# Performance work log

Hardware: AMD Instinct MI355X
Metric: run time of the kernel (lower is better)

The kernel has to match this reference:

```python
import jax, jax.numpy as jnp
import numpy as np

SEQ_LEN, INPUT_DIM, HIDDEN_DIM, OUTPUT_DIM = 512, 512, 1024, 512
BATCH = 64


def setup_inputs() -> dict:
    key = jax.random.key(0)
    k1, k2, k3, k4, k5 = jax.random.split(key, 5)
    fan_in_i2h = INPUT_DIM + HIDDEN_DIM
    s1 = 1.0 / np.sqrt(fan_in_i2h)
    s2 = 1.0 / np.sqrt(HIDDEN_DIM)
    return {
        "x": jax.random.normal(k1, (BATCH, SEQ_LEN, INPUT_DIM), dtype=jnp.float32),
        # i2h: Linear(input_dim+hidden_dim, 4*hidden_dim); stored as (in, out) for x @ W
        "W_i2h": jax.random.uniform(k2, (fan_in_i2h, 4 * HIDDEN_DIM), minval=-s1, maxval=s1, dtype=jnp.float32),
        "b_i2h": jax.random.uniform(k3, (4 * HIDDEN_DIM,), minval=-s1, maxval=s1, dtype=jnp.float32),
        # h2o: Linear(hidden_dim, output_dim)
        "W_h2o": jax.random.uniform(k4, (HIDDEN_DIM, OUTPUT_DIM), minval=-s2, maxval=s2, dtype=jnp.float32),
        "b_h2o": jax.random.uniform(k5, (OUTPUT_DIM,), minval=-s2, maxval=s2, dtype=jnp.float32),
    }


def reference(x, W_i2h, b_i2h, W_h2o, b_h2o):
    B = x.shape[0]
    H = W_h2o.shape[0]
    h0 = jnp.zeros((B, H), dtype=x.dtype)
    c0 = jnp.zeros((B, H), dtype=x.dtype)

    def step(carry, x_t):
        h_t, c_t = carry
        combined = jnp.concatenate([x_t, h_t], axis=1)  # [B, in+H]
        gates = combined @ W_i2h + b_i2h                # [B, 4H]
        i_t, f_t, g_t, o_t = jnp.split(gates, 4, axis=1)
        i_t = jax.nn.sigmoid(i_t)
        f_t = jax.nn.sigmoid(f_t)
        g_t = jnp.tanh(g_t)
        o_t = jax.nn.sigmoid(o_t)
        c_new = f_t * c_t + i_t * g_t
        h_new = o_t * jnp.tanh(c_new)
        return (h_new, c_new), None

    # scan over time: x [B, T, in] -> [T, B, in]
    (h_last, _), _ = jax.lax.scan(step, (h0, c0), jnp.swapaxes(x, 0, 1))
    # original returns only the last timestep's output projection
    return h_last @ W_h2o + b_h2o
```

## Files before the change

kernel.cpp:

```cpp
#include <hip/hip_runtime.h>
#include <hip/hip_bf16.h>
#include <stdint.h>


typedef __bf16 bf16x8 __attribute__((ext_vector_type(8)));
typedef float  f32x4  __attribute__((ext_vector_type(4)));
typedef unsigned long long u64;

#define NWG   256
#define NTHR  512

#define WS_FLAGS  0
#define WS_GOMB   1024
#define WS_HBUF   17408
#define HB_STRIDE 262144
#define HB_LO     131072
#define WS_HLAST  (WS_HBUF + 2*HB_STRIDE)

#define L_WHI   0
#define L_WLO   49152
#define L_EXCH  98304
#define L_EXCH2 102400
#define LDS_BYTES 106496

__device__ __forceinline__ float sigm(float x) {
    return __builtin_amdgcn_rcpf(1.0f + __expf(-x));
}
__device__ __forceinline__ float tanh_f(float x) {
    x = fminf(fmaxf(x, -20.0f), 20.0f);
    float e = __expf(-2.0f * x);
    return (1.0f - e) * __builtin_amdgcn_rcpf(1.0f + e);
}

__global__ void lstm_init(char* __restrict__ ws) {
    int id = blockIdx.x * 256 + threadIdx.x;
    for (int i = id; i < 69888; i += 256 * 256)
        __hip_atomic_store((unsigned*)ws + i, 0u,
                           __ATOMIC_RELAXED, __HIP_MEMORY_SCOPE_AGENT);
}

__global__ __launch_bounds__(NTHR) void lstm_main(
        const float* __restrict__ x, const float* __restrict__ Wi2h,
        const float* __restrict__ bi2h, const float* __restrict__ Wh2o,
        const float* __restrict__ bh2o, float* __restrict__ out,
        char* __restrict__ ws) {
    extern __shared__ char lds[];
    const int tid = threadIdx.x, wg = blockIdx.x;
    const int w = tid >> 6, lane = tid & 63, g = lane >> 4, nl = lane & 15;
    const int mt = w & 3, kh = w >> 2;

    for (int u = tid; u < 3072; u += NTHR) {
        int ak = u >> 4, cl = u & 15;
        int n = (cl >> 2) * 1024 + wg * 4 + (cl & 3);
        bf16x8 hi8, lo8;
#pragma unroll
        for (int j = 0; j < 8; ++j) {
            float v = Wi2h[(size_t)(ak * 8 + j) * 4096 + n];
            __bf16 h = (__bf16)v;
            hi8[j] = h;
            lo8[j] = (__bf16)(v - (float)h);
        }
        *(bf16x8*)(lds + L_WHI + (size_t)u * 16) = hi8;
        *(bf16x8*)(lds + L_WLO + (size_t)u * 16) = lo8;
    }
    const float bias_nl = bi2h[(nl >> 2) * 1024 + wg * 4 + (nl & 3)];
    __syncthreads();

    unsigned* flags = (unsigned*)(ws + WS_FLAGS);
    unsigned* my_mb = (unsigned*)(ws + WS_GOMB) + wg * 16;
    float* exch  = (float*)(lds + L_EXCH);
    float* exch2 = (float*)(lds + L_EXCH2);
    float creg = 0.f;

#pragma unroll 1
    for (int t = 0; t < 512; ++t) {
        const char* hb_rd = ws + WS_HBUF + (size_t)(t & 1) * HB_STRIDE;
        char*       hb_wr = ws + WS_HBUF + (size_t)((t + 1) & 1) * HB_STRIDE;
        f32x4 acc0 = {0.f, 0.f, 0.f, 0.f}, acc1 = {0.f, 0.f, 0.f, 0.f};

        {
            const float* xb = x + ((size_t)(mt * 16 + nl) * 512 + t) * 512 + g * 8;
            const int s0 = kh * 8;
#pragma unroll
            for (int si = 0; si < 8; ++si) {
                const int s = s0 + si;
                float4 v0 = *(const float4*)(xb + s * 32);
                float4 v1 = *(const float4*)(xb + s * 32 + 4);
                float vv[8] = {v0.x, v0.y, v0.z, v0.w, v1.x, v1.y, v1.z, v1.w};
                bf16x8 ahi, alo;
#pragma unroll
                for (int j = 0; j < 8; ++j) {
                    __bf16 h = (__bf16)vv[j];
                    ahi[j] = h;
                    alo[j] = (__bf16)(vv[j] - (float)h);
                }
                const char* bp = lds + (size_t)(4 * s + g) * 256 + nl * 16;
                bf16x8 bhi = *(const bf16x8*)(bp + L_WHI);
                bf16x8 blo = *(const bf16x8*)(bp + L_WLO);
                if (s & 1) {
                    acc1 = __builtin_amdgcn_mfma_f32_16x16x32_bf16(ahi, bhi, acc1, 0, 0, 0);
                    acc1 = __builtin_amdgcn_mfma_f32_16x16x32_bf16(ahi, blo, acc1, 0, 0, 0);
                    acc1 = __builtin_amdgcn_mfma_f32_16x16x32_bf16(alo, bhi, acc1, 0, 0, 0);
                } else {
                    acc0 = __builtin_amdgcn_mfma_f32_16x16x32_bf16(ahi, bhi, acc0, 0, 0, 0);
                    acc0 = __builtin_amdgcn_mfma_f32_16x16x32_bf16(ahi, blo, acc0, 0, 0, 0);
                    acc0 = __builtin_amdgcn_mfma_f32_16x16x32_bf16(alo, bhi, acc0, 0, 0, 0);
                }
            }
        }

        if (tid == 0) {
            while (__hip_atomic_load(my_mb, __ATOMIC_RELAXED,
                                     __HIP_MEMORY_SCOPE_AGENT) < (unsigned)t) {}
        }
        __syncthreads();

        {
            const int s0 = 16 + kh * 16;
#pragma unroll 8
            for (int si = 0; si < 16; ++si) {
                const int s = s0 + si;
                size_t ha = ((size_t)(mt * 32 + (s - 16)) * 64 + lane) * 16;
                const char* bse = hb_rd + ha;
                u64 q0 = __hip_atomic_load((const u64*)(bse),
                           __ATOMIC_RELAXED, __HIP_MEMORY_SCOPE_AGENT);
                u64 q1 = __hip_atomic_load((const u64*)(bse + 8),
                           __ATOMIC_RELAXED, __HIP_MEMORY_SCOPE_AGENT);
                u64 q2 = __hip_atomic_load((const u64*)(bse + HB_LO),
                           __ATOMIC_RELAXED, __HIP_MEMORY_SCOPE_AGENT);
                u64 q3 = __hip_atomic_load((const u64*)(bse + HB_LO + 8),
                           __ATOMIC_RELAXED, __HIP_MEMORY_SCOPE_AGENT);
                union { u64 q[2]; bf16x8 v; } uh, ul;
                uh.q[0] = q0; uh.q[1] = q1;
                ul.q[0] = q2; ul.q[1] = q3;
                bf16x8 ahi = uh.v, alo = ul.v;
                const char* bp = lds + (size_t)(4 * s + g) * 256 + nl * 16;
                bf16x8 bhi = *(const bf16x8*)(bp + L_WHI);
                bf16x8 blo = *(const bf16x8*)(bp + L_WLO);
                if (s & 1) {
                    acc1 = __builtin_amdgcn_mfma_f32_16x16x32_bf16(ahi, bhi, acc1, 0, 0, 0);
                    acc1 = __builtin_amdgcn_mfma_f32_16x16x32_bf16(ahi, blo, acc1, 0, 0, 0);
                    acc1 = __builtin_amdgcn_mfma_f32_16x16x32_bf16(alo, bhi, acc1, 0, 0, 0);
                } else {
                    acc0 = __builtin_amdgcn_mfma_f32_16x16x32_bf16(ahi, bhi, acc0, 0, 0, 0);
                    acc0 = __builtin_amdgcn_mfma_f32_16x16x32_bf16(ahi, blo, acc0, 0, 0, 0);
                    acc0 = __builtin_amdgcn_mfma_f32_16x16x32_bf16(alo, bhi, acc0, 0, 0, 0);
                }
            }
        }

        if (kh == 1) {
#pragma unroll
            for (int j = 0; j < 4; ++j)
                exch[mt * 256 + (g * 4 + j) * 16 + nl] = acc0[j] + acc1[j];
        }
        __syncthreads();
        if (kh == 0) {
#pragma unroll
            for (int j = 0; j < 4; ++j) {
                float pre = acc0[j] + acc1[j] + exch[mt * 256 + (g * 4 + j) * 16 + nl]
                          + bias_nl;
                float act = ((nl >> 2) == 2) ? tanh_f(pre) : sigm(pre);
                exch2[mt * 256 + (g * 4 + j) * 16 + nl] = act;
            }
        }
        __syncthreads();
        if (tid < 256) {
            int mt2 = tid >> 6, r = (tid >> 2) & 15, hc = tid & 3;
            const float* a2 = exch2 + mt2 * 256 + r * 16;
            float iv = a2[hc], fv = a2[4 + hc], gv = a2[8 + hc], ov = a2[12 + hc];
            float cc = fv * creg + iv * gv;
            creg = cc;
            float hv = ov * tanh_f(cc);
            __bf16 hh = (__bf16)hv;
            __bf16 hl = (__bf16)(hv - (float)hh);
            int k = 512 + wg * 4 + hc;
            int hs = (k >> 5) - 16, kg = (k >> 3) & 3, j8 = k & 7;
            uint32_t ad = ((uint32_t)(mt2 * 32 + hs) * 64 + kg * 16 + r) * 16 + j8 * 2;
            __hip_atomic_store((unsigned short*)(hb_wr + ad),
                               __builtin_bit_cast(unsigned short, hh),
                               __ATOMIC_RELAXED, __HIP_MEMORY_SCOPE_AGENT);
            __hip_atomic_store((unsigned short*)(hb_wr + HB_LO + ad),
                               __builtin_bit_cast(unsigned short, hl),
                               __ATOMIC_RELAXED, __HIP_MEMORY_SCOPE_AGENT);
            if (t == 511)
                __hip_atomic_store((float*)(ws + WS_HLAST)
                                       + (mt2 * 16 + r) * 1024 + wg * 4 + hc, hv,
                                   __ATOMIC_RELAXED, __HIP_MEMORY_SCOPE_AGENT);
        }
        __syncthreads();
        if (tid == 0)
            __hip_atomic_store(&flags[wg], (unsigned)(t + 1),
                               __ATOMIC_RELAXED, __HIP_MEMORY_SCOPE_AGENT);
        if (wg == 0 && w == 0) {
            unsigned tgt = (unsigned)(t + 1);
            const u64* f64 = (const u64*)flags;
            for (;;) {
                u64 a = __hip_atomic_load(f64 + 2 * lane,
                          __ATOMIC_RELAXED, __HIP_MEMORY_SCOPE_AGENT);
                u64 b = __hip_atomic_load(f64 + 2 * lane + 1,
                          __ATOMIC_RELAXED, __HIP_MEMORY_SCOPE_AGENT);
                unsigned m0 = min(min((unsigned)a, (unsigned)(a >> 32)),
                                  min((unsigned)b, (unsigned)(b >> 32)));
                if (__all(m0 >= tgt)) break;
            }
            unsigned* mb = (unsigned*)(ws + WS_GOMB);
#pragma unroll
            for (int q = 0; q < 4; ++q)
                __hip_atomic_store(mb + (q * 64 + lane) * 16, tgt,
                                   __ATOMIC_RELAXED, __HIP_MEMORY_SCOPE_AGENT);
        }
    }

    if (tid == 0) {
        while (__hip_atomic_load(my_mb, __ATOMIC_RELAXED,
                                 __HIP_MEMORY_SCOPE_AGENT) < 512u) {}
    }
    __syncthreads();
    __builtin_amdgcn_fence(__ATOMIC_ACQUIRE, "agent");

    const float* HL = (const float*)(ws + WS_HLAST);
    float* hl = (float*)lds;
    float* pp = (float*)(lds + 8192);
    int bb = wg & 63, q = wg >> 6;
    hl[tid]       = HL[bb * 1024 + tid];
    hl[tid + 512] = HL[bb * 1024 + 512 + tid];
    __syncthreads();
    int c = q * 128 + (tid & 127), kq = tid >> 7;
    const float* wc = Wh2o + c;
    float part = 0.f;
#pragma unroll 8
    for (int k = kq * 256; k < kq * 256 + 256; ++k)
        part += hl[k] * wc[(size_t)k * 512];
    pp[kq * 128 + (tid & 127)] = part;
    __syncthreads();
    if (tid < 128)
        out[bb * 512 + q * 128 + tid] =
            pp[tid] + pp[128 + tid] + pp[256 + tid] + pp[384 + tid] + bh2o[q * 128 + tid];
}

extern "C" void kernel_launch(void* const* d_in, const int* in_sizes, int n_in,
                              void* d_out, int out_size, void* d_ws, size_t ws_size,
                              hipStream_t stream) {
    const float* x    = (const float*)d_in[0];
    const float* Wi2h = (const float*)d_in[1];
    const float* bi2h = (const float*)d_in[2];
    const float* Wh2o = (const float*)d_in[3];
    const float* bh2o = (const float*)d_in[4];
    float* out = (float*)d_out;
    char* ws = (char*)d_ws;

    hipFuncSetAttribute(reinterpret_cast<const void*>(lstm_main),
                        hipFuncAttributeMaxDynamicSharedMemorySize, LDS_BYTES);

    lstm_init<<<256, 256, 0, stream>>>(ws);

    void* args[] = {(void*)&x, (void*)&Wi2h, (void*)&bi2h, (void*)&Wh2o,
                    (void*)&bh2o, (void*)&out, (void*)&ws};
    hipLaunchCooperativeKernel(reinterpret_cast<void*>(lstm_main),
                               dim3(NWG), dim3(NTHR), args, LDS_BYTES, stream);
}
```

Before: 5.293 ms.

## Stage recurrent h state per-XCD with cooperative copy and pipelined loads

Each workgroup finds its XCC id and a slot within that XCD. Per step, the 32 workgroups on an XCD each copy a slice of the global h buffer into an XCD-local staging buffer, then synchronise through a per-XCD counter and flag. The MFMA pass then reads h from the staging buffer with sc0 loads issued in software-pipelined batches, and half of the x-projection work is moved between the copy and the wait to hide latency. This aims to cut cross-XCD coherent traffic for h reads, at the cost of an extra per-XCD barrier, and it assumes exactly 32 workgroups land on each XCD.

```diff
diff --git a/kernel.cpp b/kernel.cpp
--- a/kernel.cpp
+++ b/kernel.cpp
@@ -10,12 +10,17 @@
 #define NWG   256
 #define NTHR  512
 
-#define WS_FLAGS  0
-#define WS_GOMB   1024
-#define WS_HBUF   17408
-#define HB_STRIDE 262144
-#define HB_LO     131072
-#define WS_HLAST  (WS_HBUF + 2*HB_STRIDE)
+#define WS_FLAGS   0
+#define WS_GOMB    1024
+#define WS_XCDC    17408
+#define WS_SCNT    17920
+#define WS_SFLAG   18432
+#define WS_HBUF    20480
+#define HB_STRIDE  262144
+#define HB_LO      131072
+#define WS_HLAST   544768
+#define WS_STAGE   806912
+#define STG_STRIDE 262144
 
 #define L_WHI   0
 #define L_WLO   49152
@@ -34,12 +39,77 @@
 
 __global__ void lstm_init(char* __restrict__ ws) {
     int id = blockIdx.x * 256 + threadIdx.x;
-    for (int i = id; i < 69888; i += 256 * 256)
+    for (int i = id; i < 136192; i += 256 * 256)
         __hip_atomic_store((unsigned*)ws + i, 0u,
                            __ATOMIC_RELAXED, __HIP_MEMORY_SCOPE_AGENT);
 }
 
-__global__ __launch_bounds__(NTHR) void lstm_main(
+#define X_HALF(A)                                                              \
+  { _Pragma("unroll")                                                          \
+    for (int si = (A); si < (A) + 4; ++si) {                                   \
+      const int s = kh * 8 + si;                                               \
+      float4 v0 = *(const float4*)(xb + s * 32);                               \
+      float4 v1 = *(const float4*)(xb + s * 32 + 4);                           \
+      float vv[8] = {v0.x, v0.y, v0.z, v0.w, v1.x, v1.y, v1.z, v1.w};          \
+      bf16x8 ahi, alo;                                                         \
+      _Pragma("unroll")                                                        \
+      for (int j = 0; j < 8; ++j) {                                            \
+        __bf16 hh_ = (__bf16)vv[j];                                            \
+        ahi[j] = hh_;                                                          \
+        alo[j] = (__bf16)(vv[j] - (float)hh_);                                 \
+      }                                                                        \
+      const char* bp = lds + (size_t)(4 * s + g) * 256 + nl * 16;              \
+      bf16x8 bhi = *(const bf16x8*)(bp + L_WHI);                               \
+      bf16x8 blo = *(const bf16x8*)(bp + L_WLO);                               \
+      if (si & 1) {                                                            \
+        acc1 = __builtin_amdgcn_mfma_f32_16x16x32_bf16(ahi, bhi, acc1, 0, 0, 0);\
+        acc1 = __builtin_amdgcn_mfma_f32_16x16x32_bf16(ahi, blo, acc1, 0, 0, 0);\
+        acc1 = __builtin_amdgcn_mfma_f32_16x16x32_bf16(alo, bhi, acc1, 0, 0, 0);\
+      } else {                                                                 \
+        acc0 = __builtin_amdgcn_mfma_f32_16x16x32_bf16(ahi, bhi, acc0, 0, 0, 0);\
+        acc0 = __builtin_amdgcn_mfma_f32_16x16x32_bf16(ahi, blo, acc0, 0, 0, 0);\
+        acc0 = __builtin_amdgcn_mfma_f32_16x16x32_bf16(alo, bhi, acc0, 0, 0, 0);\
+      }                                                                        \
+    } }
+
+#define ISSUE(B)                                                               \
+  { _Pragma("unroll")                                                          \
+    for (int si = 4 * (B); si < 4 * (B) + 4; ++si) {                           \
+      uint64_t a0 = (uint64_t)(sb + habase + si * 1024);                       \
+      asm volatile("global_load_dwordx4 %0, %1, off sc0"                       \
+                   : "=v"(vh[si]) : "v"(a0) : "memory");                       \
+      uint64_t a1 = a0 + 131072;                                               \
+      asm volatile("global_load_dwordx4 %0, %1, off sc0"                       \
+                   : "=v"(vl[si]) : "v"(a1) : "memory");                       \
+    } }
+
+#define WAITV(N)                                                               \
+  do { asm volatile("s_waitcnt vmcnt(" #N ")" ::: "memory");                   \
+       __builtin_amdgcn_sched_barrier(0); } while (0)
+
+#define COMPB(B)                                                               \
+  { _Pragma("unroll")                                                          \
+    for (int si = 4 * (B); si < 4 * (B) + 4; ++si) {                           \
+      union UU { float4 f; bf16x8 b; };                                        \
+      UU uh, ul;                                                               \
+      uh.f = vh[si];                                                           \
+      ul.f = vl[si];                                                           \
+      bf16x8 ahi = uh.b, alo = ul.b;                                           \
+      const char* bp = lds + (size_t)(64 + kh * 64 + 4 * si + g) * 256 + nl * 16;\
+      bf16x8 bhi = *(const bf16x8*)(bp + L_WHI);                               \
+      bf16x8 blo = *(const bf16x8*)(bp + L_WLO);                               \
+      if (si & 1) {                                                            \
+        acc1 = __builtin_amdgcn_mfma_f32_16x16x32_bf16(ahi, bhi, acc1, 0, 0, 0);\
+        acc1 = __builtin_amdgcn_mfma_f32_16x16x32_bf16(ahi, blo, acc1, 0, 0, 0);\
+        acc1 = __builtin_amdgcn_mfma_f32_16x16x32_bf16(alo, bhi, acc1, 0, 0, 0);\
+      } else {                                                                 \
+        acc0 = __builtin_amdgcn_mfma_f32_16x16x32_bf16(ahi, bhi, acc0, 0, 0, 0);\
+        acc0 = __builtin_amdgcn_mfma_f32_16x16x32_bf16(ahi, blo, acc0, 0, 0, 0);\
+        acc0 = __builtin_amdgcn_mfma_f32_16x16x32_bf16(alo, bhi, acc0, 0, 0, 0);\
+      }                                                                        \
+    } }
+
+__global__ __launch_bounds__(NTHR, 2) void lstm_main(
         const float* __restrict__ x, const float* __restrict__ Wi2h,
         const float* __restrict__ bi2h, const float* __restrict__ Wh2o,
         const float* __restrict__ bh2o, float* __restrict__ out,
@@ -66,6 +136,18 @@
     const float bias_nl = bi2h[(nl >> 2) * 1024 + wg * 4 + (nl & 3)];
     __syncthreads();
 
+    unsigned xcc;
+    asm("s_getreg_b32 %0, hwreg(HW_REG_XCC_ID)" : "=s"(xcc));
+    if (tid == 0) {
+        unsigned sl = __hip_atomic_fetch_add((unsigned*)(ws + WS_XCDC) + xcc * 16,
+                                             1u, __ATOMIC_RELAXED,
+                                             __HIP_MEMORY_SCOPE_AGENT);
+        *(unsigned*)(lds + L_EXCH) = sl;
+    }
+    __syncthreads();
+    const unsigned slot = *(volatile unsigned*)(lds + L_EXCH);
+    __syncthreads();
+
     unsigned* flags = (unsigned*)(ws + WS_FLAGS);
     unsigned* my_mb = (unsigned*)(ws + WS_GOMB) + wg * 16;
     float* exch  = (float*)(lds + L_EXCH);
@@ -76,38 +158,11 @@
     for (int t = 0; t < 512; ++t) {
         const char* hb_rd = ws + WS_HBUF + (size_t)(t & 1) * HB_STRIDE;
         char*       hb_wr = ws + WS_HBUF + (size_t)((t + 1) & 1) * HB_STRIDE;
+        char* sbuf = ws + WS_STAGE + ((size_t)xcc * 2 + (t & 1)) * STG_STRIDE;
         f32x4 acc0 = {0.f, 0.f, 0.f, 0.f}, acc1 = {0.f, 0.f, 0.f, 0.f};
-
-        {
-            const float* xb = x + ((size_t)(mt * 16 + nl) * 512 + t) * 512 + g * 8;
-            const int s0 = kh * 8;
-#pragma unroll
-            for (int si = 0; si < 8; ++si) {
-                const int s = s0 + si;
-                float4 v0 = *(const float4*)(xb + s * 32);
-                float4 v1 = *(const float4*)(xb + s * 32 + 4);
-                float vv[8] = {v0.x, v0.y, v0.z, v0.w, v1.x, v1.y, v1.z, v1.w};
-                bf16x8 ahi, alo;
-#pragma unroll
-                for (int j = 0; j < 8; ++j) {
-                    __bf16 h = (__bf16)vv[j];
-                    ahi[j] = h;
-                    alo[j] = (__bf16)(vv[j] - (float)h);
-                }
-                const char* bp = lds + (size_t)(4 * s + g) * 256 + nl * 16;
-                bf16x8 bhi = *(const bf16x8*)(bp + L_WHI);
-                bf16x8 blo = *(const bf16x8*)(bp + L_WLO);
-                if (s & 1) {
-                    acc1 = __builtin_amdgcn_mfma_f32_16x16x32_bf16(ahi, bhi, acc1, 0, 0, 0);
-                    acc1 = __builtin_amdgcn_mfma_f32_16x16x32_bf16(ahi, blo, acc1, 0, 0, 0);
-                    acc1 = __builtin_amdgcn_mfma_f32_16x16x32_bf16(alo, bhi, acc1, 0, 0, 0);
-                } else {
-                    acc0 = __builtin_amdgcn_mfma_f32_16x16x32_bf16(ahi, bhi, acc0, 0, 0, 0);
-                    acc0 = __builtin_amdgcn_mfma_f32_16x16x32_bf16(ahi, blo, acc0, 0, 0, 0);
-                    acc0 = __builtin_amdgcn_mfma_f32_16x16x32_bf16(alo, bhi, acc0, 0, 0, 0);
-                }
-            }
-        }
+        const float* xb = x + ((size_t)(mt * 16 + nl) * 512 + t) * 512 + g * 8;
+
+        X_HALF(0)
 
         if (tid == 0) {
             while (__hip_atomic_load(my_mb, __ATOMIC_RELAXED,
@@ -116,37 +171,51 @@
         __syncthreads();
 
         {
-            const int s0 = 16 + kh * 16;
-#pragma unroll 8
-            for (int si = 0; si < 16; ++si) {
-                const int s = s0 + si;
-                size_t ha = ((size_t)(mt * 32 + (s - 16)) * 64 + lane) * 16;
-                const char* bse = hb_rd + ha;
-                u64 q0 = __hip_atomic_load((const u64*)(bse),
-                           __ATOMIC_RELAXED, __HIP_MEMORY_SCOPE_AGENT);
-                u64 q1 = __hip_atomic_load((const u64*)(bse + 8),
-                           __ATOMIC_RELAXED, __HIP_MEMORY_SCOPE_AGENT);
-                u64 q2 = __hip_atomic_load((const u64*)(bse + HB_LO),
-                           __ATOMIC_RELAXED, __HIP_MEMORY_SCOPE_AGENT);
-                u64 q3 = __hip_atomic_load((const u64*)(bse + HB_LO + 8),
-                           __ATOMIC_RELAXED, __HIP_MEMORY_SCOPE_AGENT);
-                union { u64 q[2]; bf16x8 v; } uh, ul;
-                uh.q[0] = q0; uh.q[1] = q1;
-                ul.q[0] = q2; ul.q[1] = q3;
-                bf16x8 ahi = uh.v, alo = ul.v;
-                const char* bp = lds + (size_t)(4 * s + g) * 256 + nl * 16;
-                bf16x8 bhi = *(const bf16x8*)(bp + L_WHI);
-                bf16x8 blo = *(const bf16x8*)(bp + L_WLO);
-                if (s & 1) {
-                    acc1 = __builtin_amdgcn_mfma_f32_16x16x32_bf16(ahi, bhi, acc1, 0, 0, 0);
-                    acc1 = __builtin_amdgcn_mfma_f32_16x16x32_bf16(ahi, blo, acc1, 0, 0, 0);
-                    acc1 = __builtin_amdgcn_mfma_f32_16x16x32_bf16(alo, bhi, acc1, 0, 0, 0);
-                } else {
-                    acc0 = __builtin_amdgcn_mfma_f32_16x16x32_bf16(ahi, bhi, acc0, 0, 0, 0);
-                    acc0 = __builtin_amdgcn_mfma_f32_16x16x32_bf16(ahi, blo, acc0, 0, 0, 0);
-                    acc0 = __builtin_amdgcn_mfma_f32_16x16x32_bf16(alo, bhi, acc0, 0, 0, 0);
-                }
-            }
+            uint32_t soff = slot * 8192 + (uint32_t)tid * 16;
+            const char* sin = hb_rd + soff;
+            union { u64 q[2]; float4 v; } sv;
+            sv.q[0] = __hip_atomic_load((const u64*)sin, __ATOMIC_RELAXED,
+                                        __HIP_MEMORY_SCOPE_AGENT);
+            sv.q[1] = __hip_atomic_load((const u64*)(sin + 8), __ATOMIC_RELAXED,
+                                        __HIP_MEMORY_SCOPE_AGENT);
+            *(float4*)(sbuf + soff) = sv.v;
+        }
+        __syncthreads();
+        if (tid == 0) {
+            unsigned c = __hip_atomic_fetch_add((unsigned*)(ws + WS_SCNT) + xcc * 16,
+                                                1u, __ATOMIC_RELAXED,
+                                                __HIP_MEMORY_SCOPE_AGENT);
+            if (c == 32u * (unsigned)(t + 1) - 1u)
+                __hip_atomic_store((unsigned*)(ws + WS_SFLAG) + xcc * 16,
+                                   (unsigned)(t + 1), __ATOMIC_RELAXED,
+                                   __HIP_MEMORY_SCOPE_AGENT);
+        }
+
+        X_HALF(4)
+
+        if (tid == 0) {
+            const unsigned* sf = (const unsigned*)(ws + WS_SFLAG) + xcc * 16;
+            while (__hip_atomic_load(sf, __ATOMIC_RELAXED,
+                                     __HIP_MEMORY_SCOPE_AGENT) < (unsigned)(t + 1)) {}
+        }
+        __syncthreads();
+
+        {
+            const char* sb = sbuf;
+            const uint32_t habase = ((uint32_t)(mt * 32 + kh * 16) * 64 + lane) * 16;
+            float4 vh[16], vl[16];
+            ISSUE(0)
+            ISSUE(1)
+            WAITV(8);
+            COMPB(0)
+            ISSUE(2)
+            WAITV(8);
+            COMPB(1)
+            ISSUE(3)
+            WAITV(8);
+            COMPB(2)
+            WAITV(0);
+            COMPB(3)
         }
 
         if (kh == 1) {
```

Result: faster. 4.515 ms (-14.7%).
